# Performance work log

Hardware: AMD Instinct MI355X
Metric: run time of the kernel (lower is better)

## Reference

```python
import jax, jax.numpy as jnp
import numpy as np

D_MODEL = 1024
HEADS = 16
DIM_HEAD = 64
INNER = HEADS * DIM_HEAD


def setup_inputs() -> dict:
    key = jax.random.key(0)
    ks = jax.random.split(key, 5)
    B, N = 4, 2048
    x = jax.random.normal(ks[0], (B, N, D_MODEL), dtype=jnp.float32)
    w_qkv = jax.random.normal(ks[1], (INNER * 3, D_MODEL), dtype=jnp.float32) * (1.0 / np.sqrt(D_MODEL))
    b_qkv = jax.random.normal(ks[2], (INNER * 3,), dtype=jnp.float32) * 0.02
    w_out = jax.random.normal(ks[3], (D_MODEL, INNER), dtype=jnp.float32) * (1.0 / np.sqrt(INNER))
    logit_scale = jnp.log(10.0 * jnp.ones((HEADS, 1, 1), dtype=jnp.float32))
    return {"x": x, "w_qkv": w_qkv, "b_qkv": b_qkv, "w_out": w_out, "logit_scale": logit_scale}


def _l2norm(t, eps=1e-12):
    # matches F.normalize(dim=-1): x / max(||x||, eps)
    n = jnp.sqrt(jnp.sum(t * t, axis=-1, keepdims=True))
    return t / jnp.maximum(n, eps)


def reference(x, w_qkv, b_qkv, w_out, logit_scale):
    B, N, C = x.shape
    qkv = x @ w_qkv.T + b_qkv                      # [B,N,3*INNER]
    qkv = qkv.reshape(B, N, 3, HEADS, DIM_HEAD)
    qkv = jnp.transpose(qkv, (2, 0, 3, 1, 4))       # [3,B,H,N,Dh]
    q, k, v = qkv[0], qkv[1], qkv[2]
    attn = jnp.einsum('bhnd,bhmd->bhnm', _l2norm(q), _l2norm(k))
    scale = jnp.exp(jnp.minimum(logit_scale, jnp.log(1.0 / 0.01)))  # [H,1,1]
    attn = attn * scale[None]                       # broadcast over batch
    attn = jax.nn.softmax(attn, axis=-1)
    out = jnp.einsum('bhnm,bhmd->bhnd', attn, v)    # [B,H,N,Dh]
    out = jnp.transpose(out, (0, 2, 1, 3)).reshape(B, N, C)
    return out @ w_out.T
```

## Files before the change

### kernel.cpp

```cpp
#include <hip/hip_runtime.h>

typedef __attribute__((ext_vector_type(8))) __bf16 bf16x8;
typedef __attribute__((ext_vector_type(4))) float f32x4;
typedef unsigned short u16;

__device__ __forceinline__ u16 f2bf(float f) {
    union { float f; unsigned u; } v; v.f = f;
    unsigned r = v.u + 0x7FFFu + ((v.u >> 16) & 1u);
    return (u16)(r >> 16);
}
__device__ __forceinline__ float bf2f(u16 h) {
    union { unsigned u; float f; } v; v.u = ((unsigned)h) << 16;
    return v.f;
}
__device__ __forceinline__ u16 f2bf_n(float f) {
    union { __bf16 b; u16 u; } t; t.b = (__bf16)f; return t.u;
}
__device__ __forceinline__ bf16x8 ld_bf16x8(const u16* p) {
    union { uint4 u; bf16x8 b; } t;
    t.u = *(const uint4*)p;
    return t.b;
}
__device__ __forceinline__ void async16(const void* g, const void* l) {
    __builtin_amdgcn_global_load_lds((const __attribute__((address_space(1))) void*)g,
                                     (__attribute__((address_space(3))) void*)l, 16, 0, 0);
}

#define BATCH 4
#define NSEQ 2048
#define HEADS 16
#define DH 64
#define DMODEL 1024
#define MROWS 8192
#define NQKV 3072

__global__ void split_bf16(const float* __restrict__ src, u16* __restrict__ hi,
                           u16* __restrict__ lo, int n) {
    int i = blockIdx.x * blockDim.x + threadIdx.x;
    if (i < n) {
        float f = src[i];
        u16 h = f2bf(f);
        hi[i] = h;
        lo[i] = f2bf(f - bf2f(h));
    }
}
__global__ void cvt_bf16(const float* __restrict__ src, u16* __restrict__ dst, int n) {
    int i = blockIdx.x * blockDim.x + threadIdx.x;
    if (i < n) dst[i] = f2bf(src[i]);
}

__global__ __launch_bounds__(256) void qkv_gemm(
    const u16* __restrict__ A,
    const u16* __restrict__ Bh, const u16* __restrict__ Bl,
    const float* __restrict__ bias,
    u16* __restrict__ Qn, u16* __restrict__ Kn, u16* __restrict__ Vt) {
    const int K = DMODEL, TK = 32;
    __shared__ __align__(16) u16 sA[128 * 32];
    __shared__ __align__(16) u16 sBh[128 * 32], sBl[128 * 32];
    const int tid = threadIdx.x, wave = tid >> 6, lane = tid & 63;
    const int quad = lane >> 4, l16 = lane & 15;
    const int m0 = blockIdx.x * 128, n0 = blockIdx.y * 128;
    const int wm = (wave & 1) * 64, wn = (wave >> 1) * 64;
    f32x4 acc[4][4] = {};

    for (int k0 = 0; k0 < K; k0 += TK) {
        __syncthreads();
        #pragma unroll
        for (int pass = 0; pass < 2; ++pass) {
            const int c = pass * 256 + tid;
            const int row = c >> 2, part = c & 3;
            const int ldsOff = (pass * 256 + wave * 64) * 16;
            const size_t ga = (size_t)(m0 + row) * K + k0 + part * 8;
            const size_t gb = (size_t)(n0 + row) * K + k0 + part * 8;
            async16(A + ga, (const char*)sA + ldsOff);
            async16(Bh + gb, (const char*)sBh + ldsOff);
            async16(Bl + gb, (const char*)sBl + ldsOff);
        }
        __syncthreads();
        bf16x8 a[4];
        #pragma unroll
        for (int mt = 0; mt < 4; ++mt)
            a[mt] = ld_bf16x8(&sA[(wm + mt * 16 + l16) * TK + quad * 8]);
        #pragma unroll
        for (int nt = 0; nt < 4; ++nt) {
            const int cix = wn + nt * 16 + l16;
            bf16x8 bh = ld_bf16x8(&sBh[cix * TK + quad * 8]);
            bf16x8 bl = ld_bf16x8(&sBl[cix * TK + quad * 8]);
            #pragma unroll
            for (int mt = 0; mt < 4; ++mt) {
                acc[mt][nt] = __builtin_amdgcn_mfma_f32_16x16x32_bf16(a[mt], bh, acc[mt][nt], 0, 0, 0);
                acc[mt][nt] = __builtin_amdgcn_mfma_f32_16x16x32_bf16(a[mt], bl, acc[mt][nt], 0, 0, 0);
            }
        }
    }

    #pragma unroll
    for (int nt = 0; nt < 4; ++nt) {
        const float bv = bias[n0 + wn + nt * 16 + l16];
        #pragma unroll
        for (int mt = 0; mt < 4; ++mt)
            #pragma unroll
            for (int r = 0; r < 4; ++r)
                acc[mt][nt][r] += bv;
    }

    if (n0 < 2048) {
        u16* dst = (n0 < 1024) ? Qn : Kn;
        const int nq = (n0 & 1023) + wn;
        const int hh = nq >> 6;
        #pragma unroll
        for (int mt = 0; mt < 4; ++mt) {
            float ss[4] = {};
            #pragma unroll
            for (int nt = 0; nt < 4; ++nt)
                #pragma unroll
                for (int r = 0; r < 4; ++r)
                    ss[r] += acc[mt][nt][r] * acc[mt][nt][r];
            #pragma unroll
            for (int r = 0; r < 4; ++r) {
                ss[r] += __shfl_xor(ss[r], 1);
                ss[r] += __shfl_xor(ss[r], 2);
                ss[r] += __shfl_xor(ss[r], 4);
                ss[r] += __shfl_xor(ss[r], 8);
                ss[r] = 1.f / fmaxf(sqrtf(ss[r]), 1e-12f);
            }
            const int mbase = m0 + wm + mt * 16 + quad * 4;
            const int b = mbase >> 11, n = mbase & 2047;
            #pragma unroll
            for (int r = 0; r < 4; ++r) {
                size_t rowoff = (((size_t)(b * HEADS + hh)) * NSEQ + n + r) * DH;
                #pragma unroll
                for (int nt = 0; nt < 4; ++nt)
                    dst[rowoff + nt * 16 + l16] = f2bf_n(acc[mt][nt][r] * ss[r]);
            }
        }
    } else {
        const int nv = (n0 - 2048) + wn;
        const int hh = nv >> 6;
        #pragma unroll
        for (int nt = 0; nt < 4; ++nt) {
            const int d = nt * 16 + l16;
            #pragma unroll
            for (int mt = 0; mt < 4; ++mt) {
                const int mbase = m0 + wm + mt * 16 + quad * 4;
                const int b = mbase >> 11, n = mbase & 2047;
                ushort4 t;
                t.x = f2bf_n(acc[mt][nt][0]);
                t.y = f2bf_n(acc[mt][nt][1]);
                t.z = f2bf_n(acc[mt][nt][2]);
                t.w = f2bf_n(acc[mt][nt][3]);
                *(ushort4*)&Vt[(((size_t)(b * HEADS + hh)) * DH + d) * NSEQ + n] = t;
            }
        }
    }
}

__global__ __launch_bounds__(256) void out_gemm(
    const u16* __restrict__ A, const u16* __restrict__ B, float* __restrict__ C) {
    const int K = DMODEL, N = DMODEL, TK = 32;
    __shared__ __align__(16) u16 sA[128 * 32], sB[128 * 32];
    const int tid = threadIdx.x, wave = tid >> 6, lane = tid & 63;
    const int quad = lane >> 4, l16 = lane & 15;
    const int m0 = blockIdx.x * 128, n0 = blockIdx.y * 128;
    const int wm = (wave & 1) * 64, wn = (wave >> 1) * 64;
    f32x4 acc[4][4] = {};

    for (int k0 = 0; k0 < K; k0 += TK) {
        __syncthreads();
        #pragma unroll
        for (int pass = 0; pass < 2; ++pass) {
            const int c = pass * 256 + tid;
            const int row = c >> 2, part = c & 3;
            const int ldsOff = (pass * 256 + wave * 64) * 16;
            const size_t ga = (size_t)(m0 + row) * K + k0 + part * 8;
            const size_t gb = (size_t)(n0 + row) * K + k0 + part * 8;
            async16(A + ga, (const char*)sA + ldsOff);
            async16(B + gb, (const char*)sB + ldsOff);
        }
        __syncthreads();
        bf16x8 a[4];
        #pragma unroll
        for (int mt = 0; mt < 4; ++mt)
            a[mt] = ld_bf16x8(&sA[(wm + mt * 16 + l16) * TK + quad * 8]);
        #pragma unroll
        for (int nt = 0; nt < 4; ++nt) {
            bf16x8 b = ld_bf16x8(&sB[(wn + nt * 16 + l16) * TK + quad * 8]);
            #pragma unroll
            for (int mt = 0; mt < 4; ++mt)
                acc[mt][nt] = __builtin_amdgcn_mfma_f32_16x16x32_bf16(a[mt], b, acc[mt][nt], 0, 0, 0);
        }
    }
    #pragma unroll
    for (int nt = 0; nt < 4; ++nt) {
        const int n = n0 + wn + nt * 16 + l16;
        #pragma unroll
        for (int mt = 0; mt < 4; ++mt) {
            const int mbase = m0 + wm + mt * 16 + quad * 4;
            #pragma unroll
            for (int r = 0; r < 4; ++r)
                C[(size_t)(mbase + r) * N + n] = acc[mt][nt][r];
        }
    }
}

__global__ __launch_bounds__(512) void flash_attn(
    const u16* __restrict__ Q, const u16* __restrict__ Kn, const u16* __restrict__ Vt,
    const float* __restrict__ lsc, u16* __restrict__ AO) {
    const int bh = blockIdx.x;
    const int q0 = blockIdx.y * 128;
    const int h = bh & (HEADS - 1), b = bh >> 4;
    const int tid = threadIdx.x, wave = tid >> 6, lane = tid & 63;
    const int quad = lane >> 4, l16 = lane & 15;
    const float scale = __expf(fminf(lsc[h], 4.6051702f));
    const float c1 = scale * 1.4426950408889634f;

    __shared__ __align__(16) u16 Ks[64][72];
    __shared__ __align__(16) u16 Vs[64][72];
    __shared__ __align__(16) u16 Ps[8][16][68];

    const u16* qbase = Q + ((size_t)bh * NSEQ + q0 + wave * 16) * DH;
    bf16x8 qa[2];
    qa[0] = ld_bf16x8(qbase + l16 * DH + quad * 8);
    qa[1] = ld_bf16x8(qbase + l16 * DH + 32 + quad * 8);

    f32x4 O[4] = {};
    float lr[4] = {0.f, 0.f, 0.f, 0.f};

    const u16* kb = Kn + (size_t)bh * NSEQ * DH;
    const u16* vb = Vt + (size_t)bh * DH * NSEQ;

    for (int kt = 0; kt < NSEQ; kt += 64) {
        __syncthreads();
        {
            int row = tid >> 3, part = tid & 7;
            *(uint4*)&Ks[row][part * 8] = *(const uint4*)(kb + (size_t)(kt + row) * DH + part * 8);
            *(uint4*)&Vs[row][part * 8] = *(const uint4*)(vb + (size_t)row * NSEQ + kt + part * 8);
        }
        __syncthreads();

        f32x4 S[4] = {};
        #pragma unroll
        for (int nt = 0; nt < 4; ++nt) {
            bf16x8 k0 = ld_bf16x8(&Ks[nt * 16 + l16][quad * 8]);
            bf16x8 k1 = ld_bf16x8(&Ks[nt * 16 + l16][32 + quad * 8]);
            S[nt] = __builtin_amdgcn_mfma_f32_16x16x32_bf16(qa[0], k0, S[nt], 0, 0, 0);
            S[nt] = __builtin_amdgcn_mfma_f32_16x16x32_bf16(qa[1], k1, S[nt], 0, 0, 0);
        }

        #pragma unroll
        for (int nt = 0; nt < 4; ++nt) {
            #pragma unroll
            for (int r = 0; r < 4; ++r) {
                float pv = __builtin_amdgcn_exp2f(__builtin_fmaf(S[nt][r], c1, -c1));
                lr[r] += pv;
                Ps[wave][quad * 4 + r][nt * 16 + l16] = f2bf_n(pv);
            }
        }
        asm volatile("s_waitcnt lgkmcnt(0)" ::: "memory");
        bf16x8 pa0 = ld_bf16x8(&Ps[wave][l16][quad * 8]);
        bf16x8 pa1 = ld_bf16x8(&Ps[wave][l16][32 + quad * 8]);

        #pragma unroll
        for (int dt = 0; dt < 4; ++dt) {
            bf16x8 v0 = ld_bf16x8(&Vs[dt * 16 + l16][quad * 8]);
            bf16x8 v1 = ld_bf16x8(&Vs[dt * 16 + l16][32 + quad * 8]);
            O[dt] = __builtin_amdgcn_mfma_f32_16x16x32_bf16(pa0, v0, O[dt], 0, 0, 0);
            O[dt] = __builtin_amdgcn_mfma_f32_16x16x32_bf16(pa1, v1, O[dt], 0, 0, 0);
        }
    }

    #pragma unroll
    for (int r = 0; r < 4; ++r) {
        float s = lr[r];
        s += __shfl_xor(s, 1);
        s += __shfl_xor(s, 2);
        s += __shfl_xor(s, 4);
        s += __shfl_xor(s, 8);
        lr[r] = fmaxf(s, 1e-30f);
    }

    #pragma unroll
    for (int r = 0; r < 4; ++r) {
        float inv = 1.f / lr[r];
        size_t row = (size_t)b * NSEQ + q0 + wave * 16 + quad * 4 + r;
        #pragma unroll
        for (int dt = 0; dt < 4; ++dt)
            AO[row * DMODEL + h * DH + dt * 16 + l16] = f2bf_n(O[dt][r] * inv);
    }
}

extern "C" void kernel_launch(void* const* d_in, const int* in_sizes, int n_in,
                              void* d_out, int out_size, void* d_ws, size_t ws_size,
                              hipStream_t stream) {
    const float* x    = (const float*)d_in[0];
    const float* wqkv = (const float*)d_in[1];
    const float* bqkv = (const float*)d_in[2];
    const float* wout = (const float*)d_in[3];
    const float* lsc  = (const float*)d_in[4];

    char* ws = (char*)d_ws;
    u16* xb   = (u16*)(ws + 0);
    u16* wqh  = (u16*)(ws + 16777216);
    u16* wql  = (u16*)(ws + 23068672);
    u16* wob  = (u16*)(ws + 29360128);
    u16* qn   = (u16*)(ws + 31457280);
    u16* kn   = (u16*)(ws + 48234496);
    u16* vt   = (u16*)(ws + 65011712);
    u16* ao   = xb;

    cvt_bf16<<<MROWS * DMODEL / 256, 256, 0, stream>>>(x, xb, MROWS * DMODEL);
    split_bf16<<<NQKV * DMODEL / 256, 256, 0, stream>>>(wqkv, wqh, wql, NQKV * DMODEL);
    cvt_bf16<<<DMODEL * DMODEL / 256, 256, 0, stream>>>(wout, wob, DMODEL * DMODEL);

    qkv_gemm<<<dim3(MROWS / 128, NQKV / 128), 256, 0, stream>>>(xb, wqh, wql, bqkv, qn, kn, vt);
    flash_attn<<<dim3(BATCH * HEADS, NSEQ / 128), 512, 0, stream>>>(qn, kn, vt, lsc, ao);
    out_gemm<<<dim3(MROWS / 128, DMODEL / 128), 256, 0, stream>>>(ao, wob, (float*)d_out);
}
```

Baseline: 414.2 us.

## Prefetch next K/V tile into registers and add MFMA priority hints in flash attention

Software-pipelines the flash-attention K/V loads. The next 64-key tile is loaded into registers before the current tile is computed, using a two-stage A/B register rotation with explicit vmcnt/lgkmcnt waits and raw barriers, so global-load latency overlaps with MFMA work. Wraps the MFMA sections in s_setprio raises and pads the P staging buffer rows from 68 to 72 elements. The cost is more registers per thread and one wasted wrap-around load on the final iteration.

```diff
diff --git a/kernel.cpp b/kernel.cpp
--- a/kernel.cpp
+++ b/kernel.cpp
@@ -216,7 +216,7 @@
 
     __shared__ __align__(16) u16 Ks[64][72];
     __shared__ __align__(16) u16 Vs[64][72];
-    __shared__ __align__(16) u16 Ps[8][16][68];
+    __shared__ __align__(16) u16 Ps[8][16][72];
 
     const u16* qbase = Q + ((size_t)bh * NSEQ + q0 + wave * 16) * DH;
     bf16x8 qa[2];
@@ -226,19 +226,17 @@
     f32x4 O[4] = {};
     float lr[4] = {0.f, 0.f, 0.f, 0.f};
 
-    const u16* kb = Kn + (size_t)bh * NSEQ * DH;
-    const u16* vb = Vt + (size_t)bh * DH * NSEQ;
-
-    for (int kt = 0; kt < NSEQ; kt += 64) {
-        __syncthreads();
-        {
-            int row = tid >> 3, part = tid & 7;
-            *(uint4*)&Ks[row][part * 8] = *(const uint4*)(kb + (size_t)(kt + row) * DH + part * 8);
-            *(uint4*)&Vs[row][part * 8] = *(const uint4*)(vb + (size_t)row * NSEQ + kt + part * 8);
-        }
-        __syncthreads();
-
+    const int row = tid >> 3, part = tid & 7;
+    const u16* kb = Kn + (size_t)bh * NSEQ * DH + (size_t)row * DH + part * 8;
+    const u16* vb = Vt + (size_t)bh * DH * NSEQ + (size_t)row * NSEQ + part * 8;
+
+    uint4 kA = *(const uint4*)kb;
+    uint4 vA = *(const uint4*)vb;
+    uint4 kB, vB;
+
+    auto compute = [&]() {
         f32x4 S[4] = {};
+        __builtin_amdgcn_s_setprio(1);
         #pragma unroll
         for (int nt = 0; nt < 4; ++nt) {
             bf16x8 k0 = ld_bf16x8(&Ks[nt * 16 + l16][quad * 8]);
@@ -246,6 +244,7 @@
             S[nt] = __builtin_amdgcn_mfma_f32_16x16x32_bf16(qa[0], k0, S[nt], 0, 0, 0);
             S[nt] = __builtin_amdgcn_mfma_f32_16x16x32_bf16(qa[1], k1, S[nt], 0, 0, 0);
         }
+        __builtin_amdgcn_s_setprio(0);
 
         #pragma unroll
         for (int nt = 0; nt < 4; ++nt) {
@@ -260,6 +259,7 @@
         bf16x8 pa0 = ld_bf16x8(&Ps[wave][l16][quad * 8]);
         bf16x8 pa1 = ld_bf16x8(&Ps[wave][l16][32 + quad * 8]);
 
+        __builtin_amdgcn_s_setprio(1);
         #pragma unroll
         for (int dt = 0; dt < 4; ++dt) {
             bf16x8 v0 = ld_bf16x8(&Vs[dt * 16 + l16][quad * 8]);
@@ -267,6 +267,35 @@
             O[dt] = __builtin_amdgcn_mfma_f32_16x16x32_bf16(pa0, v0, O[dt], 0, 0, 0);
             O[dt] = __builtin_amdgcn_mfma_f32_16x16x32_bf16(pa1, v1, O[dt], 0, 0, 0);
         }
+        __builtin_amdgcn_s_setprio(0);
+    };
+
+    #pragma unroll 1
+    for (int kt = 0; kt < NSEQ; kt += 128) {
+        asm volatile("s_waitcnt lgkmcnt(0)" ::: "memory");
+        __builtin_amdgcn_s_barrier();
+        kB = *(const uint4*)(kb + (size_t)(kt + 64) * DH);
+        vB = *(const uint4*)(vb + (kt + 64));
+        asm volatile("s_waitcnt vmcnt(2)" ::: "memory");
+        *(uint4*)&Ks[row][part * 8] = kA;
+        *(uint4*)&Vs[row][part * 8] = vA;
+        asm volatile("s_waitcnt lgkmcnt(0)" ::: "memory");
+        __builtin_amdgcn_s_barrier();
+        compute();
+
+        asm volatile("s_waitcnt lgkmcnt(0)" ::: "memory");
+        __builtin_amdgcn_s_barrier();
+        {
+            const int nk = (kt + 128) < NSEQ ? (kt + 128) : 0;
+            kA = *(const uint4*)(kb + (size_t)nk * DH);
+            vA = *(const uint4*)(vb + nk);
+        }
+        asm volatile("s_waitcnt vmcnt(2)" ::: "memory");
+        *(uint4*)&Ks[row][part * 8] = kB;
+        *(uint4*)&Vs[row][part * 8] = vB;
+        asm volatile("s_waitcnt lgkmcnt(0)" ::: "memory");
+        __builtin_amdgcn_s_barrier();
+        compute();
     }
 
     #pragma unroll
@@ -282,10 +311,10 @@
     #pragma unroll
     for (int r = 0; r < 4; ++r) {
         float inv = 1.f / lr[r];
-        size_t row = (size_t)b * NSEQ + q0 + wave * 16 + quad * 4 + r;
+        size_t orow = (size_t)b * NSEQ + q0 + wave * 16 + quad * 4 + r;
         #pragma unroll
         for (int dt = 0; dt < 4; ++dt)
-            AO[row * DMODEL + h * DH + dt * 16 + l16] = f2bf_n(O[dt][r] * inv);
+            AO[orow * DMODEL + h * DH + dt * 16 + l16] = f2bf_n(O[dt][r] * inv);
     }
 }
 
```

After: 357.9 us. 1.16x faster.
